# Performance work log

Hardware: AMD Instinct MI355X
Metric: run time of the kernel (lower is better)

Reference implementation:

```python
import jax, jax.numpy as jnp
import numpy as np

NHEADS = 8
START_ID = 1
MAX_LEN = 24

def _ln(x, g, b, eps=1e-5):
    m = x.mean(-1, keepdims=True)
    v = ((x - m) ** 2).mean(-1, keepdims=True)
    return (x - m) * jax.lax.rsqrt(v + eps) * g + b

def _mha(q_in, kv_in, w, b, ow, ob, mask):
    # q_in: [Lq,B,E], kv_in: [Lk,B,E]; w: [E,3E] packed q/k/v (transposed torch in_proj)
    E = q_in.shape[-1]; H = NHEADS; D = E // H
    Lq, B = q_in.shape[0], q_in.shape[1]; Lk = kv_in.shape[0]
    q = (q_in @ w[:, :E] + b[:E]).reshape(Lq, B, H, D)
    k = (kv_in @ w[:, E:2 * E] + b[E:2 * E]).reshape(Lk, B, H, D)
    v = (kv_in @ w[:, 2 * E:] + b[2 * E:]).reshape(Lk, B, H, D)
    s = jnp.einsum('qbhd,kbhd->bhqk', q, k) * (1.0 / float(np.sqrt(D)))
    if mask is not None:
        s = s + mask
    a = jax.nn.softmax(s, axis=-1)
    o = jnp.einsum('bhqk,kbhd->qbhd', a, v).reshape(Lq, B, E)
    return o @ ow + ob

def _sinusoidal_pe(S, E):
    pos = np.arange(S)[:, None]
    div = np.exp(np.arange(0, E, 2) * (-np.log(10000.0) / E))
    pe = np.zeros((S, E), dtype=np.float32)
    pe[:, 0::2] = np.sin(pos * div)
    pe[:, 1::2] = np.cos(pos * div)
    return jnp.asarray(pe)[:, None, :]  # [S,1,E]

def _model(input_tensor, emb, enc_attn_w, enc_attn_b, enc_attn_ow, enc_attn_ob,
           enc_ln1_g, enc_ln1_b, enc_ln2_g, enc_ln2_b,
           enc_ffn_w1, enc_ffn_b1, enc_ffn_w2, enc_ffn_b2,
           enc_norm_g, enc_norm_b,
           dec_sa_w, dec_sa_b, dec_sa_ow, dec_sa_ob,
           dec_ca_w, dec_ca_b, dec_ca_ow, dec_ca_ob,
           dec_ln1_g, dec_ln1_b, dec_ln2_g, dec_ln2_b, dec_ln3_g, dec_ln3_b,
           dec_ffn_w1, dec_ffn_b1, dec_ffn_w2, dec_ffn_b2,
           dec_norm_g, dec_norm_b, voc_w, voc_b):
    E = emb.shape[1]
    B, S = input_tensor.shape
    # encoder: seq-first [S,B,E], sinusoidal PE added (decoder side gets NO PE, as in source)
    x = jnp.take(emb, input_tensor.T, axis=0) + _sinusoidal_pe(S, E)
    for l in range(enc_attn_w.shape[0]):  # post-LN encoder layers
        a = _mha(x, x, enc_attn_w[l], enc_attn_b[l], enc_attn_ow[l], enc_attn_ob[l], None)
        x = _ln(x + a, enc_ln1_g[l], enc_ln1_b[l])
        f = jax.nn.relu(x @ enc_ffn_w1[l] + enc_ffn_b1[l]) @ enc_ffn_w2[l] + enc_ffn_b2[l]
        x = _ln(x + f, enc_ln2_g[l], enc_ln2_b[l])
    memory = _ln(x, enc_norm_g, enc_norm_b)

    Lbuf = MAX_LEN + 1
    causal = jnp.where(jnp.triu(jnp.ones((Lbuf, Lbuf), jnp.float32), k=1) == 1, -jnp.inf, 0.0)

    def dec_forward(tokens):
        # full (wasteful, KV-cache-free) decoder pass over the whole token buffer,
        # matching the source's recompute-everything greedy loop; causal masking
        # makes position i identical to the source's length-(i+1) prefix pass.
        y = jnp.take(emb, tokens, axis=0)  # [Lbuf,B,E]; shared embedding, no PE (as in source)
        for l in range(dec_sa_w.shape[0]):
            a = _mha(y, y, dec_sa_w[l], dec_sa_b[l], dec_sa_ow[l], dec_sa_ob[l], causal)
            y = _ln(y + a, dec_ln1_g[l], dec_ln1_b[l])
            c = _mha(y, memory, dec_ca_w[l], dec_ca_b[l], dec_ca_ow[l], dec_ca_ob[l], None)
            y = _ln(y + c, dec_ln2_g[l], dec_ln2_b[l])
            f = jax.nn.relu(y @ dec_ffn_w1[l] + dec_ffn_b1[l]) @ dec_ffn_w2[l] + dec_ffn_b2[l]
            y = _ln(y + f, dec_ln3_g[l], dec_ln3_b[l])
        return _ln(y, dec_norm_g, dec_norm_b)

    def step(tokens, i):
        out_i = jnp.take(dec_forward(tokens), i, axis=0)  # [B,E] == out[-1] of prefix pass
        prob = out_i @ voc_w + voc_b                      # [B,V_tgt]
        nxt = jnp.argmax(prob, axis=-1).astype(tokens.dtype)
        return tokens.at[i + 1].set(nxt), (nxt, prob)

    tokens0 = jnp.full((Lbuf, B), START_ID, dtype=input_tensor.dtype)
    _, (pred_tokens, dists) = jax.lax.scan(step, tokens0, jnp.arange(MAX_LEN))
    return pred_tokens, dists  # [MAX_LEN,B] int, [MAX_LEN,B,V_tgt]


def setup_inputs() -> dict:
    V, VT, E, F, LE, LD, B, S = 32000, 32000, 512, 2048, 3, 3, 8, 24
    keys = iter(jax.random.split(jax.random.key(0), 48))
    def W(*shape):
        return jax.random.normal(next(keys), shape, jnp.float32) * 0.02
    return dict(
        input_tensor=jax.random.randint(next(keys), (B, S), 0, V),
        emb=W(V, E),
        enc_attn_w=W(LE, E, 3 * E), enc_attn_b=jnp.zeros((LE, 3 * E)),
        enc_attn_ow=W(LE, E, E), enc_attn_ob=jnp.zeros((LE, E)),
        enc_ln1_g=jnp.ones((LE, E)), enc_ln1_b=jnp.zeros((LE, E)),
        enc_ln2_g=jnp.ones((LE, E)), enc_ln2_b=jnp.zeros((LE, E)),
        enc_ffn_w1=W(LE, E, F), enc_ffn_b1=jnp.zeros((LE, F)),
        enc_ffn_w2=W(LE, F, E), enc_ffn_b2=jnp.zeros((LE, E)),
        enc_norm_g=jnp.ones((E,)), enc_norm_b=jnp.zeros((E,)),
        dec_sa_w=W(LD, E, 3 * E), dec_sa_b=jnp.zeros((LD, 3 * E)),
        dec_sa_ow=W(LD, E, E), dec_sa_ob=jnp.zeros((LD, E)),
        dec_ca_w=W(LD, E, 3 * E), dec_ca_b=jnp.zeros((LD, 3 * E)),
        dec_ca_ow=W(LD, E, E), dec_ca_ob=jnp.zeros((LD, E)),
        dec_ln1_g=jnp.ones((LD, E)), dec_ln1_b=jnp.zeros((LD, E)),
        dec_ln2_g=jnp.ones((LD, E)), dec_ln2_b=jnp.zeros((LD, E)),
        dec_ln3_g=jnp.ones((LD, E)), dec_ln3_b=jnp.zeros((LD, E)),
        dec_ffn_w1=W(LD, E, F), dec_ffn_b1=jnp.zeros((LD, F)),
        dec_ffn_w2=W(LD, F, E), dec_ffn_b2=jnp.zeros((LD, E)),
        dec_norm_g=jnp.ones((E,)), dec_norm_b=jnp.zeros((E,)),
        voc_w=W(E, VT), voc_b=jnp.zeros((VT,)),
    )


def reference(input_tensor, emb, enc_attn_w, enc_attn_b, enc_attn_ow, enc_attn_ob,
              enc_ln1_g, enc_ln1_b, enc_ln2_g, enc_ln2_b,
              enc_ffn_w1, enc_ffn_b1, enc_ffn_w2, enc_ffn_b2,
              enc_norm_g, enc_norm_b,
              dec_sa_w, dec_sa_b, dec_sa_ow, dec_sa_ob,
              dec_ca_w, dec_ca_b, dec_ca_ow, dec_ca_ob,
              dec_ln1_g, dec_ln1_b, dec_ln2_g, dec_ln2_b, dec_ln3_g, dec_ln3_b,
              dec_ffn_w1, dec_ffn_b1, dec_ffn_w2, dec_ffn_b2,
              dec_norm_g, dec_norm_b, voc_w, voc_b):
    return _model(input_tensor, emb, enc_attn_w, enc_attn_b, enc_attn_ow, enc_attn_ob,
                  enc_ln1_g, enc_ln1_b, enc_ln2_g, enc_ln2_b,
                  enc_ffn_w1, enc_ffn_b1, enc_ffn_w2, enc_ffn_b2,
                  enc_norm_g, enc_norm_b,
                  dec_sa_w, dec_sa_b, dec_sa_ow, dec_sa_ob,
                  dec_ca_w, dec_ca_b, dec_ca_ow, dec_ca_ob,
                  dec_ln1_g, dec_ln1_b, dec_ln2_g, dec_ln2_b, dec_ln3_g, dec_ln3_b,
                  dec_ffn_w1, dec_ffn_b1, dec_ffn_w2, dec_ffn_b2,
                  dec_norm_g, dec_norm_b, voc_w, voc_b)
```

## Files before the change

kernel.cpp:

```cpp
#include <hip/hip_runtime.h>
#include <stdint.h>

#define E    512
#define H    8
#define DH   64
#define BB   8
#define SS   24
#define FF   2048
#define NL   3
#define VTOK 32000
#define LBUF 25
#define ML   24
#define START_ID 1

__global__ void enc_embed_kernel(const int* __restrict__ inp, const float* __restrict__ emb,
                                 float* __restrict__ x) {
  int r = blockIdx.x;
  int s = r / BB, b = r % BB;
  int tok = inp[b * SS + s];
  const float* er = emb + (size_t)tok * E;
  for (int e = threadIdx.x; e < E; e += blockDim.x) {
    int j = e >> 1;
    double dv = exp(-((double)(2 * j)) * (log(10000.0) / (double)E));
    double ang = (double)s * dv;
    double pe = (e & 1) ? cos(ang) : sin(ang);
    x[(size_t)r * E + e] = er[e] + (float)pe;
  }
}

__device__ __forceinline__ void ln_tile(float* Al, const float* __restrict__ g,
                                        const float* __restrict__ b,
                                        float* rm, float* rrs) {
  int t = threadIdx.x;
  int rr = t >> 5, q = t & 31;
  const float* ar = Al + rr * 512;
  float sm = 0.f, s2 = 0.f;
  for (int j = q; j < 512; j += 32) { float v = ar[j]; sm += v; s2 += v * v; }
  for (int off = 16; off; off >>= 1) {
    sm += __shfl_down(sm, off, 32);
    s2 += __shfl_down(s2, off, 32);
  }
  if (q == 0) {
    float m = sm * (1.0f / 512.0f);
    float var = s2 * (1.0f / 512.0f) - m * m;
    rm[rr] = m;
    rrs[rr] = 1.0f / sqrtf(var + 1e-5f);
  }
  __syncthreads();
  for (int idx = t; idx < 4096; idx += 256) {
    int r2 = idx >> 9, c2 = idx & 511;
    Al[idx] = (Al[idx] - rm[r2]) * rrs[r2] * g[c2] + b[c2];
  }
  __syncthreads();
}

__global__ __launch_bounds__(256) void fgemm_kernel(
    const float* __restrict__ A, int K,
    const float* __restrict__ W, int ldw, int N,
    const float* __restrict__ bias,
    const float* __restrict__ resid,
    float* __restrict__ C, int relu,
    unsigned long long* __restrict__ amax,
    const float* __restrict__ lng, const float* __restrict__ lnb,
    const float* __restrict__ lng2, const float* __restrict__ lnb2,
    float* __restrict__ astore,
    const int* __restrict__ gtok, const float* __restrict__ gemb,
    const float* __restrict__ rpart, const float* __restrict__ rbias,
    const float* __restrict__ rresid) {
  __shared__ float Al[8 * 512];
  __shared__ float red[16 * 512];
  __shared__ float rm[8], rrs[8];
  int t = threadIdx.x;
  int c0 = blockIdx.x * 64;
  int s = blockIdx.y;
  int row0 = blockIdx.z * 8;
  int kbase = s * 512;
  if (gtok) {
    for (int i = t; i < 1024; i += 256) {
      int r = i >> 7, cc = i & 127;
      int tok = gtok[r];
      ((float4*)Al)[i] = *(const float4*)(gemb + (size_t)tok * E + (cc << 2));
    }
  } else if (rpart) {
    for (int i = t; i < 1024; i += 256) {
      int r = i >> 7, cc = i & 127;
      int c = cc << 2;
      float4 v = *(const float4*)(rbias + c);
      float4 rv = *(const float4*)(rresid + (size_t)r * E + c);
      v.x += rv.x; v.y += rv.y; v.z += rv.z; v.w += rv.w;
      for (int sl = 0; sl < 4; ++sl) {
        float4 pv = *(const float4*)(rpart + ((size_t)sl * 8 + r) * E + c);
        v.x += pv.x; v.y += pv.y; v.z += pv.z; v.w += pv.w;
      }
      ((float4*)Al)[i] = v;
    }
  } else {
    for (int i = t; i < 1024; i += 256) {
      int r = i >> 7, cc = i & 127;
      ((float4*)Al)[i] = *(const float4*)(A + (size_t)(row0 + r) * K + kbase + (cc << 2));
    }
  }
  __syncthreads();
  if (lng) {
    ln_tile(Al, lng, lnb, rm, rrs);
    if (lng2) ln_tile(Al, lng2, lnb2, rm, rrs);
  }
  if (astore && blockIdx.x == 0 && blockIdx.y == 0) {
    float* ap = astore + (size_t)row0 * 512;
    for (int idx = t; idx < 4096; idx += 256) ap[idx] = Al[idx];
  }
  int tc = t & 15, tk = t >> 4;
  int col = c0 + (tc << 2);
  float acc[8][4];
#pragma unroll
  for (int m = 0; m < 8; ++m) { acc[m][0] = acc[m][1] = acc[m][2] = acc[m][3] = 0.f; }
  const float4* wp = (const float4*)(W + (size_t)kbase * ldw + col);
  const size_t ld4 = (size_t)(ldw >> 2);
#pragma unroll 8
  for (int i = 0; i < 32; ++i) {
    int k = tk + (i << 4);
    float4 wv = wp[(size_t)k * ld4];
#pragma unroll
    for (int m = 0; m < 8; ++m) {
      float a = Al[m * 512 + k];
      acc[m][0] += a * wv.x; acc[m][1] += a * wv.y;
      acc[m][2] += a * wv.z; acc[m][3] += a * wv.w;
    }
  }
#pragma unroll
  for (int m = 0; m < 8; ++m) {
    float4* rr2 = (float4*)&red[tk * 512 + m * 64 + (tc << 2)];
    *rr2 = make_float4(acc[m][0], acc[m][1], acc[m][2], acc[m][3]);
  }
  __syncthreads();
  float out2[2];
#pragma unroll
  for (int j = 0; j < 2; ++j) {
    int o = t + j * 256;
    float v = 0.f;
#pragma unroll
    for (int sl = 0; sl < 16; ++sl) v += red[sl * 512 + o];
    out2[j] = v;
  }
  int S = gridDim.y;
  if (S > 1) {
    int M = gridDim.z * 8;
#pragma unroll
    for (int j = 0; j < 2; ++j) {
      int o = t + j * 256; int m = o >> 6, cc = o & 63;
      C[((size_t)s * M + row0 + m) * N + c0 + cc] = out2[j];
    }
  } else {
#pragma unroll
    for (int j = 0; j < 2; ++j) {
      int o = t + j * 256; int m = o >> 6, cc = o & 63;
      int col2 = c0 + cc;
      float v = out2[j] + bias[col2];
      if (resid) v += resid[(size_t)(row0 + m) * N + col2];
      if (relu) v = fmaxf(v, 0.0f);
      C[(size_t)(row0 + m) * N + col2] = v;
      out2[j] = v;
    }
    if (amax) {
      __syncthreads();
      unsigned long long* keys = (unsigned long long*)red;
#pragma unroll
      for (int j = 0; j < 2; ++j) {
        int o = t + j * 256;
        unsigned int fb = __float_as_uint(out2[j]);
        fb = (fb & 0x80000000u) ? ~fb : (fb | 0x80000000u);
        int col2 = c0 + (o & 63);
        keys[o] = ((unsigned long long)fb << 32) |
                  (unsigned long long)(0xFFFFFFFFu - (unsigned)col2);
      }
      __syncthreads();
      if (t < 64) {
        for (int m = 0; m < 8; ++m) {
          unsigned long long k = keys[m * 64 + t];
          for (int off = 32; off; off >>= 1) {
            unsigned long long o2 = __shfl_down(k, off);
            if (o2 > k) k = o2;
          }
          if (t == 0) atomicMax(&amax[m], k);
        }
      }
    }
  }
}

__global__ __launch_bounds__(256) void reduce_br_kernel(const float* __restrict__ part, int S, int M,
                                 const float* __restrict__ bias,
                                 const float* __restrict__ resid,
                                 float* __restrict__ outp) {
  int r = blockIdx.x, t = threadIdx.x;
#pragma unroll
  for (int j = 0; j < 2; ++j) {
    int c = t + j * 256;
    float v = bias[c] + resid[(size_t)r * E + c];
    for (int s = 0; s < S; ++s) v += part[((size_t)s * M + r) * E + c];
    outp[(size_t)r * E + c] = v;
  }
}

__global__ __launch_bounds__(256) void reduce_ln_kernel(const float* __restrict__ part, int S,
                                 const float* __restrict__ bias,
                                 const float* __restrict__ resid,
                                 const float* __restrict__ g, const float* __restrict__ bta,
                                 float* __restrict__ out) {
  int b = blockIdx.x, t = threadIdx.x;
  float v0 = bias[t] + resid[(size_t)b * E + t];
  float v1 = bias[t + 256] + resid[(size_t)b * E + t + 256];
  for (int s = 0; s < S; ++s) {
    v0 += part[((size_t)s * 8 + b) * E + t];
    v1 += part[((size_t)s * 8 + b) * E + t + 256];
  }
  __shared__ float red[256];
  red[t] = v0 + v1;
  __syncthreads();
  for (int s = 128; s > 0; s >>= 1) { if (t < s) red[t] += red[t + s]; __syncthreads(); }
  float m = red[0] * (1.0f / (float)E);
  __syncthreads();
  float d0 = v0 - m, d1 = v1 - m;
  red[t] = d0 * d0 + d1 * d1;
  __syncthreads();
  for (int s = 128; s > 0; s >>= 1) { if (t < s) red[t] += red[t + s]; __syncthreads(); }
  float v = red[0] * (1.0f / (float)E);
  float rstd = 1.0f / sqrtf(v + 1e-5f);
  out[(size_t)b * E + t]       = d0 * rstd * g[t]       + bta[t];
  out[(size_t)b * E + t + 256] = d1 * rstd * g[t + 256] + bta[t + 256];
}

__global__ void enc_attn_kernel(const float* __restrict__ qkv, float* __restrict__ o) {
  int b = blockIdx.x >> 3, h = blockIdx.x & 7;
  __shared__ float qs[SS * DH], ks[SS * DH], vs[SS * DH];
  __shared__ float sc[SS][SS];
  int t = threadIdx.x;
  for (int idx = t; idx < SS * DH; idx += 256) {
    int srow = idx / DH, d = idx - srow * DH;
    size_t base = ((size_t)(srow * BB + b)) * (3 * E) + h * DH + d;
    qs[idx] = qkv[base];
    ks[idx] = qkv[base + E];
    vs[idx] = qkv[base + 2 * E];
  }
  __syncthreads();
  for (int p = t; p < SS * SS; p += 256) {
    int qi = p / SS, kj = p - qi * SS;
    float a = 0.f;
    for (int d = 0; d < DH; ++d) a += qs[qi * DH + d] * ks[kj * DH + d];
    sc[qi][kj] = a * 0.125f;
  }
  __syncthreads();
  if (t < SS) {
    float mx = -1e30f;
    for (int j = 0; j < SS; ++j) mx = fmaxf(mx, sc[t][j]);
    float sm = 0.f;
    for (int j = 0; j < SS; ++j) { float ev = expf(sc[t][j] - mx); sc[t][j] = ev; sm += ev; }
    float inv = 1.0f / sm;
    for (int j = 0; j < SS; ++j) sc[t][j] *= inv;
  }
  __syncthreads();
  for (int p = t; p < SS * DH; p += 256) {
    int qi = p / DH, d = p - qi * DH;
    float a = 0.f;
    for (int j = 0; j < SS; ++j) a += sc[qi][j] * vs[j * DH + d];
    o[((size_t)(qi * BB + b)) * E + h * DH + d] = a;
  }
}

__global__ __launch_bounds__(64) void dec_sa_attn_kernel(const float* __restrict__ qkv,
                                   float* __restrict__ Kc, float* __restrict__ Vc,
                                   float* __restrict__ o, int pos) {
  int b = blockIdx.x >> 3, h = blockIdx.x & 7;
  int t = threadIdx.x;
  const float* qp = qkv + (size_t)b * (3 * E) + h * DH;
  const float* kn = qp + E;
  const float* vn = qp + 2 * E;
  float* kc = Kc + ((size_t)pos * BB + b) * E + h * DH;
  float* vc = Vc + ((size_t)pos * BB + b) * E + h * DH;
  __shared__ float qs[DH];
  __shared__ float sc[32];
  kc[t] = kn[t]; vc[t] = vn[t]; qs[t] = qp[t];
  __syncthreads();
  int L = pos + 1;
  if (t < L) {
    const float* kr = (t == pos) ? kn : (Kc + ((size_t)t * BB + b) * E + h * DH);
    float a = 0.f;
#pragma unroll 8
    for (int d = 0; d < DH; ++d) a += qs[d] * kr[d];
    sc[t] = a * 0.125f;
  }
  __syncthreads();
  if (t == 0) {
    float mx = -1e30f;
    for (int j = 0; j < L; ++j) mx = fmaxf(mx, sc[j]);
    float sm = 0.f;
    for (int j = 0; j < L; ++j) { float ev = expf(sc[j] - mx); sc[j] = ev; sm += ev; }
    float inv = 1.0f / sm;
    for (int j = 0; j < L; ++j) sc[j] *= inv;
  }
  __syncthreads();
  float a = 0.f;
  for (int j = 0; j < L; ++j) {
    const float* vr = (j == pos) ? vn : (Vc + ((size_t)j * BB + b) * E + h * DH);
    a += sc[j] * vr[t];
  }
  o[(size_t)b * E + h * DH + t] = a;
}

__global__ __launch_bounds__(64) void dec_ca_attn_kernel(const float* __restrict__ q,
                                   const float* __restrict__ Km, const float* __restrict__ Vm,
                                   float* __restrict__ o) {
  int b = blockIdx.x >> 3, h = blockIdx.x & 7;
  int t = threadIdx.x;
  __shared__ float qs[DH];
  __shared__ float sc[SS];
  qs[t] = q[(size_t)b * E + h * DH + t];
  __syncthreads();
  if (t < SS) {
    const float* kr = Km + ((size_t)t * BB + b) * E + h * DH;
    float a = 0.f;
#pragma unroll 8
    for (int d = 0; d < DH; ++d) a += qs[d] * kr[d];
    sc[t] = a * 0.125f;
  }
  __syncthreads();
  if (t == 0) {
    float mx = -1e30f;
    for (int j = 0; j < SS; ++j) mx = fmaxf(mx, sc[j]);
    float sm = 0.f;
    for (int j = 0; j < SS; ++j) { float ev = expf(sc[j] - mx); sc[j] = ev; sm += ev; }
    float inv = 1.0f / sm;
    for (int j = 0; j < SS; ++j) sc[j] *= inv;
  }
  __syncthreads();
  float a = 0.f;
  for (int j = 0; j < SS; ++j) a += sc[j] * Vm[((size_t)j * BB + b) * E + h * DH + t];
  o[(size_t)b * E + h * DH + t] = a;
}

__global__ void dec_init_kernel(int* __restrict__ tokens, unsigned long long* __restrict__ amax) {
  int t = threadIdx.x;
  if (t < BB) { tokens[t] = START_ID; amax[t] = 0ull; }
}

__global__ void next_token_kernel(unsigned long long* __restrict__ amax, int* __restrict__ tokens,
                                  float* __restrict__ outtok, int i) {
  int t = threadIdx.x;
  if (t < BB) {
    unsigned long long p = amax[t];
    int idx = (int)(0xFFFFFFFFu - (unsigned int)(p & 0xFFFFFFFFull));
    tokens[(i + 1) * BB + t] = idx;
    outtok[i * BB + t] = (float)idx;
    amax[t] = 0ull;
  }
}

extern "C" void kernel_launch(void* const* d_in, const int* in_sizes, int n_in,
                              void* d_out, int out_size, void* d_ws, size_t ws_size,
                              hipStream_t stream) {
  (void)in_sizes; (void)n_in; (void)out_size; (void)ws_size;
  const int*   inp   = (const int*)d_in[0];
  const float* emb   = (const float*)d_in[1];
  const float* e_aw  = (const float*)d_in[2];
  const float* e_ab  = (const float*)d_in[3];
  const float* e_aow = (const float*)d_in[4];
  const float* e_aob = (const float*)d_in[5];
  const float* e_l1g = (const float*)d_in[6];
  const float* e_l1b = (const float*)d_in[7];
  const float* e_l2g = (const float*)d_in[8];
  const float* e_l2b = (const float*)d_in[9];
  const float* e_f1w = (const float*)d_in[10];
  const float* e_f1b = (const float*)d_in[11];
  const float* e_f2w = (const float*)d_in[12];
  const float* e_f2b = (const float*)d_in[13];
  const float* e_ng  = (const float*)d_in[14];
  const float* e_nb  = (const float*)d_in[15];
  const float* d_saw = (const float*)d_in[16];
  const float* d_sab = (const float*)d_in[17];
  const float* d_saow= (const float*)d_in[18];
  const float* d_saob= (const float*)d_in[19];
  const float* d_caw = (const float*)d_in[20];
  const float* d_cab = (const float*)d_in[21];
  const float* d_caow= (const float*)d_in[22];
  const float* d_caob= (const float*)d_in[23];
  const float* d_l1g = (const float*)d_in[24];
  const float* d_l1b = (const float*)d_in[25];
  const float* d_l2g = (const float*)d_in[26];
  const float* d_l2b = (const float*)d_in[27];
  const float* d_l3g = (const float*)d_in[28];
  const float* d_l3b = (const float*)d_in[29];
  const float* d_f1w = (const float*)d_in[30];
  const float* d_f1b = (const float*)d_in[31];
  const float* d_f2w = (const float*)d_in[32];
  const float* d_f2b = (const float*)d_in[33];
  const float* d_ng  = (const float*)d_in[34];
  const float* d_nb  = (const float*)d_in[35];
  const float* voc_w = (const float*)d_in[36];
  const float* voc_b = (const float*)d_in[37];
  float* out = (float*)d_out;

  float* p = (float*)d_ws;
  auto alloc = [&](size_t n) { float* r = p; p += n; return r; };
  float* enc_x   = alloc(192 * 512);
  float* enc_tmp = alloc(192 * 2048);
  float* enc_ao  = alloc(192 * 512);
  float* enc_raw = alloc(192 * 512);
  float* mem_k   = alloc(3 * 192 * 512);
  float* mem_v   = alloc(3 * 192 * 512);
  float* partE   = alloc(4 * 192 * 512);
  float* dqkv    = alloc(8 * 1536);
  float* y_in    = alloc(8 * 512);
  float* o_sa    = alloc(8 * 512);
  float* y1      = alloc(8 * 512);
  float* y1raw   = alloc(8 * 512);
  float* qca     = alloc(8 * 512);
  float* oca     = alloc(8 * 512);
  float* y2      = alloc(8 * 512);
  float* y2raw   = alloc(8 * 512);
  float* dmid    = alloc(8 * 2048);
  float* partD   = alloc(4 * 8 * 512);
  float* cacheK  = alloc(3 * LBUF * 8 * 512);
  float* cacheV  = alloc(3 * LBUF * 8 * 512);
  int* tokens    = (int*)alloc(LBUF * 8);
  unsigned long long* amax = (unsigned long long*)alloc(16);

#define FGZ nullptr, nullptr, nullptr, nullptr, nullptr, nullptr, nullptr, nullptr, nullptr, nullptr, nullptr

  enc_embed_kernel<<<dim3(192), dim3(256), 0, stream>>>(inp, emb, enc_x);
  for (int l = 0; l < NL; ++l) {
    const float* w  = e_aw  + (size_t)l * E * 3 * E;
    const float* bq = e_ab  + (size_t)l * 3 * E;
    if (l == 0) {
      fgemm_kernel<<<dim3(24, 1, 24), dim3(256), 0, stream>>>(
          enc_x, E, w, 3 * E, 3 * E, bq, nullptr, enc_tmp, 0, FGZ);
    } else {
      fgemm_kernel<<<dim3(24, 1, 24), dim3(256), 0, stream>>>(
          enc_raw, E, w, 3 * E, 3 * E, bq, nullptr, enc_tmp, 0,
          nullptr, e_l2g + (size_t)(l - 1) * E, e_l2b + (size_t)(l - 1) * E,
          nullptr, nullptr, enc_x,
          nullptr, nullptr, nullptr, nullptr, nullptr);
    }
    enc_attn_kernel<<<dim3(64), dim3(256), 0, stream>>>(enc_tmp, enc_ao);
    fgemm_kernel<<<dim3(8, 1, 24), dim3(256), 0, stream>>>(
        enc_ao, E, e_aow + (size_t)l * E * E, E, E, e_aob + (size_t)l * E,
        enc_x, enc_raw, 0, FGZ);
    fgemm_kernel<<<dim3(32, 1, 24), dim3(256), 0, stream>>>(
        enc_raw, E, e_f1w + (size_t)l * E * FF, FF, FF, e_f1b + (size_t)l * FF,
        nullptr, enc_tmp, 1,
        nullptr, e_l1g + (size_t)l * E, e_l1b + (size_t)l * E,
        nullptr, nullptr, enc_x,
        nullptr, nullptr, nullptr, nullptr, nullptr);
    fgemm_kernel<<<dim3(8, 4, 24), dim3(256), 0, stream>>>(
        enc_tmp, FF, e_f2w + (size_t)l * FF * E, E, E, nullptr,
        nullptr, partE, 0, FGZ);
    reduce_br_kernel<<<dim3(192), dim3(256), 0, stream>>>(
        partE, 4, 192, e_f2b + (size_t)l * E, enc_x, enc_raw);
  }

  for (int l = 0; l < NL; ++l) {
    const float* w  = d_caw + (size_t)l * E * 3 * E;
    const float* bq = d_cab + (size_t)l * 3 * E;
    fgemm_kernel<<<dim3(8, 1, 24), dim3(256), 0, stream>>>(
        enc_raw, E, w + E, 3 * E, E, bq + E, nullptr,
        mem_k + (size_t)l * 192 * 512, 0,
        nullptr, e_l2g + (size_t)2 * E, e_l2b + (size_t)2 * E,
        e_ng, e_nb, nullptr,
        nullptr, nullptr, nullptr, nullptr, nullptr);
    fgemm_kernel<<<dim3(8, 1, 24), dim3(256), 0, stream>>>(
        enc_raw, E, w + 2 * E, 3 * E, E, bq + 2 * E, nullptr,
        mem_v + (size_t)l * 192 * 512, 0,
        nullptr, e_l2g + (size_t)2 * E, e_l2b + (size_t)2 * E,
        e_ng, e_nb, nullptr,
        nullptr, nullptr, nullptr, nullptr, nullptr);
  }

  dec_init_kernel<<<dim3(1), dim3(64), 0, stream>>>(tokens, amax);
  for (int i = 0; i < ML; ++i) {
    for (int l = 0; l < NL; ++l) {
      const float* saw = d_saw + (size_t)l * E * 3 * E;
      const float* sab = d_sab + (size_t)l * 3 * E;
      const float* caw = d_caw + (size_t)l * E * 3 * E;
      const float* cab = d_cab + (size_t)l * 3 * E;
      float* Kc = cacheK + (size_t)l * LBUF * 8 * 512;
      float* Vc = cacheV + (size_t)l * LBUF * 8 * 512;

      if (l == 0) {
        fgemm_kernel<<<dim3(24, 1, 1), dim3(256), 0, stream>>>(
            nullptr, E, saw, 3 * E, 3 * E, sab, nullptr, dqkv, 0,
            nullptr, nullptr, nullptr, nullptr, nullptr, y_in,
            tokens + (size_t)i * BB, emb,
            nullptr, nullptr, nullptr);
      } else {
        fgemm_kernel<<<dim3(24, 1, 1), dim3(256), 0, stream>>>(
            nullptr, E, saw, 3 * E, 3 * E, sab, nullptr, dqkv, 0,
            nullptr, d_l3g + (size_t)(l - 1) * E, d_l3b + (size_t)(l - 1) * E,
            nullptr, nullptr, y_in,
            nullptr, nullptr,
            partD, d_f2b + (size_t)(l - 1) * E, y2);
      }
      dec_sa_attn_kernel<<<dim3(64), dim3(64), 0, stream>>>(dqkv, Kc, Vc, o_sa, i);
      fgemm_kernel<<<dim3(8, 1, 1), dim3(256), 0, stream>>>(
          o_sa, E, d_saow + (size_t)l * E * E, E, E, d_saob + (size_t)l * E,
          y_in, y1raw, 0, FGZ);
      fgemm_kernel<<<dim3(8, 1, 1), dim3(256), 0, stream>>>(
          y1raw, E, caw, 3 * E, E, cab, nullptr, qca, 0,
          nullptr, d_l1g + (size_t)l * E, d_l1b + (size_t)l * E,
          nullptr, nullptr, y1,
          nullptr, nullptr, nullptr, nullptr, nullptr);
      dec_ca_attn_kernel<<<dim3(64), dim3(64), 0, stream>>>(
          qca, mem_k + (size_t)l * 192 * 512, mem_v + (size_t)l * 192 * 512, oca);
      fgemm_kernel<<<dim3(8, 1, 1), dim3(256), 0, stream>>>(
          oca, E, d_caow + (size_t)l * E * E, E, E, d_caob + (size_t)l * E,
          y1, y2raw, 0, FGZ);
      fgemm_kernel<<<dim3(32, 1, 1), dim3(256), 0, stream>>>(
          y2raw, E, d_f1w + (size_t)l * E * FF, FF, FF, d_f1b + (size_t)l * FF,
          nullptr, dmid, 1,
          nullptr, d_l2g + (size_t)l * E, d_l2b + (size_t)l * E,
          nullptr, nullptr, y2,
          nullptr, nullptr, nullptr, nullptr, nullptr);
      fgemm_kernel<<<dim3(8, 4, 1), dim3(256), 0, stream>>>(
          dmid, FF, d_f2w + (size_t)l * FF * E, E, E, nullptr,
          nullptr, partD, 0, FGZ);
    }
    reduce_ln_kernel<<<dim3(8), dim3(256), 0, stream>>>(
        partD, 4, d_f2b + (size_t)(NL - 1) * E, y2,
        d_l3g + (size_t)(NL - 1) * E, d_l3b + (size_t)(NL - 1) * E, y_in);

    float* dist_i = out + 192 + (size_t)i * (8 * VTOK);
    fgemm_kernel<<<dim3(500, 1, 1), dim3(256), 0, stream>>>(
        y_in, E, voc_w, VTOK, VTOK, voc_b, nullptr, dist_i, 0,
        amax, d_ng, d_nb, nullptr, nullptr, nullptr,
        nullptr, nullptr, nullptr, nullptr, nullptr);
    next_token_kernel<<<dim3(1), dim3(64), 0, stream>>>(amax, tokens, out, i);
  }
#undef FGZ
}
```

Before: 6.219 ms.

## Fuse decoder attention with output projection via per-head partial sums

The decoder self- and cross-attention kernels now also apply the output projection, each head writing a partial product that the next GEMM's loader sums together with bias and residual before layernorm. This drops two fgemm launches per decoder layer and step, plus the intermediate buffers. The partial-sum loop count becomes a runtime parameter, and the fgemm inner-loop unroll rises from 8 to 16. In exchange, each attention block reads a 64x512 slice of the projection weight with only 64 blocks, so occupancy is low, and the next GEMM has to read 8 partial buffers.

```diff
diff --git a/kernel.cpp b/kernel.cpp
--- a/kernel.cpp
+++ b/kernel.cpp
@@ -66,7 +66,7 @@
     float* __restrict__ astore,
     const int* __restrict__ gtok, const float* __restrict__ gemb,
     const float* __restrict__ rpart, const float* __restrict__ rbias,
-    const float* __restrict__ rresid) {
+    const float* __restrict__ rresid, int rS) {
   __shared__ float Al[8 * 512];
   __shared__ float red[16 * 512];
   __shared__ float rm[8], rrs[8];
@@ -88,7 +88,7 @@
       float4 v = *(const float4*)(rbias + c);
       float4 rv = *(const float4*)(rresid + (size_t)r * E + c);
       v.x += rv.x; v.y += rv.y; v.z += rv.z; v.w += rv.w;
-      for (int sl = 0; sl < 4; ++sl) {
+      for (int sl = 0; sl < rS; ++sl) {
         float4 pv = *(const float4*)(rpart + ((size_t)sl * 8 + r) * E + c);
         v.x += pv.x; v.y += pv.y; v.z += pv.z; v.w += pv.w;
       }
@@ -116,7 +116,7 @@
   for (int m = 0; m < 8; ++m) { acc[m][0] = acc[m][1] = acc[m][2] = acc[m][3] = 0.f; }
   const float4* wp = (const float4*)(W + (size_t)kbase * ldw + col);
   const size_t ld4 = (size_t)(ldw >> 2);
-#pragma unroll 8
+#pragma unroll 16
   for (int i = 0; i < 32; ++i) {
     int k = tk + (i << 4);
     float4 wv = wp[(size_t)k * ld4];
@@ -267,26 +267,33 @@
   }
 }
 
-__global__ __launch_bounds__(64) void dec_sa_attn_kernel(const float* __restrict__ qkv,
-                                   float* __restrict__ Kc, float* __restrict__ Vc,
-                                   float* __restrict__ o, int pos) {
+__global__ __launch_bounds__(256) void dec_sa_part_kernel(
+    const float* __restrict__ qkv,
+    float* __restrict__ Kc, float* __restrict__ Vc, int pos,
+    const float* __restrict__ W,
+    float* __restrict__ part) {
   int b = blockIdx.x >> 3, h = blockIdx.x & 7;
   int t = threadIdx.x;
-  const float* qp = qkv + (size_t)b * (3 * E) + h * DH;
-  const float* kn = qp + E;
-  const float* vn = qp + 2 * E;
-  float* kc = Kc + ((size_t)pos * BB + b) * E + h * DH;
-  float* vc = Vc + ((size_t)pos * BB + b) * E + h * DH;
-  __shared__ float qs[DH];
+  __shared__ float qs[DH], os[DH];
   __shared__ float sc[32];
-  kc[t] = kn[t]; vc[t] = vn[t]; qs[t] = qp[t];
+  const float* base = qkv + (size_t)b * 1536 + h * DH;
+  if (t < DH) {
+    qs[t] = base[t];
+    Kc[((size_t)pos * BB + b) * E + h * DH + t] = base[512 + t];
+    Vc[((size_t)pos * BB + b) * E + h * DH + t] = base[1024 + t];
+  }
   __syncthreads();
   int L = pos + 1;
   if (t < L) {
-    const float* kr = (t == pos) ? kn : (Kc + ((size_t)t * BB + b) * E + h * DH);
+    const float4* k4 = (t == pos) ? (const float4*)(base + 512)
+                                  : (const float4*)(Kc + ((size_t)t * BB + b) * E + h * DH);
+    const float4* q4 = (const float4*)qs;
     float a = 0.f;
-#pragma unroll 8
-    for (int d = 0; d < DH; ++d) a += qs[d] * kr[d];
+#pragma unroll
+    for (int d = 0; d < 16; ++d) {
+      float4 qv = q4[d], kv = k4[d];
+      a += qv.x * kv.x + qv.y * kv.y + qv.z * kv.z + qv.w * kv.w;
+    }
     sc[t] = a * 0.125f;
   }
   __syncthreads();
@@ -299,28 +306,48 @@
     for (int j = 0; j < L; ++j) sc[j] *= inv;
   }
   __syncthreads();
-  float a = 0.f;
-  for (int j = 0; j < L; ++j) {
-    const float* vr = (j == pos) ? vn : (Vc + ((size_t)j * BB + b) * E + h * DH);
-    a += sc[j] * vr[t];
-  }
-  o[(size_t)b * E + h * DH + t] = a;
-}
-
-__global__ __launch_bounds__(64) void dec_ca_attn_kernel(const float* __restrict__ q,
-                                   const float* __restrict__ Km, const float* __restrict__ Vm,
-                                   float* __restrict__ o) {
+  if (t < DH) {
+    float a = 0.f;
+    for (int j = 0; j < L; ++j) {
+      float vv = (j == pos) ? base[1024 + t]
+                            : Vc[((size_t)j * BB + b) * E + h * DH + t];
+      a += sc[j] * vv;
+    }
+    os[t] = a;
+  }
+  __syncthreads();
+  float p0 = 0.f, p1 = 0.f;
+  const float* wr = W + (size_t)h * DH * E;
+#pragma unroll 8
+  for (int d = 0; d < DH; ++d) {
+    float o = os[d];
+    p0 += o * wr[(size_t)d * E + t];
+    p1 += o * wr[(size_t)d * E + t + 256];
+  }
+  float* pp = part + ((size_t)h * BB + b) * E;
+  pp[t] = p0; pp[t + 256] = p1;
+}
+
+__global__ __launch_bounds__(256) void dec_ca_part_kernel(
+    const float* __restrict__ q,
+    const float* __restrict__ Km, const float* __restrict__ Vm,
+    const float* __restrict__ W,
+    float* __restrict__ part) {
   int b = blockIdx.x >> 3, h = blockIdx.x & 7;
   int t = threadIdx.x;
-  __shared__ float qs[DH];
+  __shared__ float qs[DH], os[DH];
   __shared__ float sc[SS];
-  qs[t] = q[(size_t)b * E + h * DH + t];
+  if (t < DH) qs[t] = q[(size_t)b * E + h * DH + t];
   __syncthreads();
   if (t < SS) {
-    const float* kr = Km + ((size_t)t * BB + b) * E + h * DH;
+    const float4* k4 = (const float4*)(Km + ((size_t)t * BB + b) * E + h * DH);
+    const float4* q4 = (const float4*)qs;
     float a = 0.f;
-#pragma unroll 8
-    for (int d = 0; d < DH; ++d) a += qs[d] * kr[d];
+#pragma unroll
+    for (int d = 0; d < 16; ++d) {
+      float4 qv = q4[d], kv = k4[d];
+      a += qv.x * kv.x + qv.y * kv.y + qv.z * kv.z + qv.w * kv.w;
+    }
     sc[t] = a * 0.125f;
   }
   __syncthreads();
@@ -333,9 +360,23 @@
     for (int j = 0; j < SS; ++j) sc[j] *= inv;
   }
   __syncthreads();
-  float a = 0.f;
-  for (int j = 0; j < SS; ++j) a += sc[j] * Vm[((size_t)j * BB + b) * E + h * DH + t];
-  o[(size_t)b * E + h * DH + t] = a;
+  if (t < DH) {
+    float a = 0.f;
+    for (int j = 0; j < SS; ++j)
+      a += sc[j] * Vm[((size_t)j * BB + b) * E + h * DH + t];
+    os[t] = a;
+  }
+  __syncthreads();
+  float p0 = 0.f, p1 = 0.f;
+  const float* wr = W + (size_t)h * DH * E;
+#pragma unroll 8
+  for (int d = 0; d < DH; ++d) {
+    float o = os[d];
+    p0 += o * wr[(size_t)d * E + t];
+    p1 += o * wr[(size_t)d * E + t + 256];
+  }
+  float* pp = part + ((size_t)h * BB + b) * E;
+  pp[t] = p0; pp[t + 256] = p1;
 }
 
 __global__ void dec_init_kernel(int* __restrict__ tokens, unsigned long long* __restrict__ amax) {
@@ -410,21 +451,19 @@
   float* partE   = alloc(4 * 192 * 512);
   float* dqkv    = alloc(8 * 1536);
   float* y_in    = alloc(8 * 512);
-  float* o_sa    = alloc(8 * 512);
   float* y1      = alloc(8 * 512);
-  float* y1raw   = alloc(8 * 512);
+  float* y2      = alloc(8 * 512);
   float* qca     = alloc(8 * 512);
-  float* oca     = alloc(8 * 512);
-  float* y2      = alloc(8 * 512);
-  float* y2raw   = alloc(8 * 512);
   float* dmid    = alloc(8 * 2048);
   float* partD   = alloc(4 * 8 * 512);
+  float* partSA  = alloc(8 * 8 * 512);
+  float* partCA  = alloc(8 * 8 * 512);
   float* cacheK  = alloc(3 * LBUF * 8 * 512);
   float* cacheV  = alloc(3 * LBUF * 8 * 512);
   int* tokens    = (int*)alloc(LBUF * 8);
   unsigned long long* amax = (unsigned long long*)alloc(16);
 
-#define FGZ nullptr, nullptr, nullptr, nullptr, nullptr, nullptr, nullptr, nullptr, nullptr, nullptr, nullptr
+#define FGZ nullptr, nullptr, nullptr, nullptr, nullptr, nullptr, nullptr, nullptr, nullptr, nullptr, nullptr, 0
 
   enc_embed_kernel<<<dim3(192), dim3(256), 0, stream>>>(inp, emb, enc_x);
   for (int l = 0; l < NL; ++l) {
@@ -438,7 +477,7 @@
           enc_raw, E, w, 3 * E, 3 * E, bq, nullptr, enc_tmp, 0,
           nullptr, e_l2g + (size_t)(l - 1) * E, e_l2b + (size_t)(l - 1) * E,
           nullptr, nullptr, enc_x,
-          nullptr, nullptr, nullptr, nullptr, nullptr);
+          nullptr, nullptr, nullptr, nullptr, nullptr, 0);
     }
     enc_attn_kernel<<<dim3(64), dim3(256), 0, stream>>>(enc_tmp, enc_ao);
     fgemm_kernel<<<dim3(8, 1, 24), dim3(256), 0, stream>>>(
@@ -449,7 +488,7 @@
         nullptr, enc_tmp, 1,
         nullptr, e_l1g + (size_t)l * E, e_l1b + (size_t)l * E,
         nullptr, nullptr, enc_x,
-        nullptr, nullptr, nullptr, nullptr, nullptr);
+        nullptr, nullptr, nullptr, nullptr, nullptr, 0);
     fgemm_kernel<<<dim3(8, 4, 24), dim3(256), 0, stream>>>(
         enc_tmp, FF, e_f2w + (size_t)l * FF * E, E, E, nullptr,
         nullptr, partE, 0, FGZ);
@@ -465,13 +504,13 @@
         mem_k + (size_t)l * 192 * 512, 0,
         nullptr, e_l2g + (size_t)2 * E, e_l2b + (size_t)2 * E,
         e_ng, e_nb, nullptr,
-        nullptr, nullptr, nullptr, nullptr, nullptr);
+        nullptr, nullptr, nullptr, nullptr, nullptr, 0);
     fgemm_kernel<<<dim3(8, 1, 24), dim3(256), 0, stream>>>(
         enc_raw, E, w + 2 * E, 3 * E, E, bq + 2 * E, nullptr,
         mem_v + (size_t)l * 192 * 512, 0,
         nullptr, e_l2g + (size_t)2 * E, e_l2b + (size_t)2 * E,
         e_ng, e_nb, nullptr,
-        nullptr, nullptr, nullptr, nullptr, nullptr);
+        nullptr, nullptr, nullptr, nullptr, nullptr, 0);
   }
 
   dec_init_kernel<<<dim3(1), dim3(64), 0, stream>>>(tokens, amax);
@@ -489,35 +528,33 @@
             nullptr, E, saw, 3 * E, 3 * E, sab, nullptr, dqkv, 0,
             nullptr, nullptr, nullptr, nullptr, nullptr, y_in,
             tokens + (size_t)i * BB, emb,
-            nullptr, nullptr, nullptr);
+            nullptr, nullptr, nullptr, 0);
       } else {
         fgemm_kernel<<<dim3(24, 1, 1), dim3(256), 0, stream>>>(
             nullptr, E, saw, 3 * E, 3 * E, sab, nullptr, dqkv, 0,
             nullptr, d_l3g + (size_t)(l - 1) * E, d_l3b + (size_t)(l - 1) * E,
             nullptr, nullptr, y_in,
             nullptr, nullptr,
-            partD, d_f2b + (size_t)(l - 1) * E, y2);
+            partD, d_f2b + (size_t)(l - 1) * E, y2, 4);
       }
-      dec_sa_attn_kernel<<<dim3(64), dim3(64), 0, stream>>>(dqkv, Kc, Vc, o_sa, i);
+      dec_sa_part_kernel<<<dim3(64), dim3(256), 0, stream>>>(
+          dqkv, Kc, Vc, i, d_saow + (size_t)l * E * E, partSA);
       fgemm_kernel<<<dim3(8, 1, 1), dim3(256), 0, stream>>>(
-          o_sa, E, d_saow + (size_t)l * E * E, E, E, d_saob + (size_t)l * E,
-          y_in, y1raw, 0, FGZ);
-      fgemm_kernel<<<dim3(8, 1, 1), dim3(256), 0, stream>>>(
-          y1raw, E, caw, 3 * E, E, cab, nullptr, qca, 0,
+          nullptr, E, caw, 3 * E, E, cab, nullptr, qca, 0,
           nullptr, d_l1g + (size_t)l * E, d_l1b + (size_t)l * E,
           nullptr, nullptr, y1,
-          nullptr, nullptr, nullptr, nullptr, nullptr);
-      dec_ca_attn_kernel<<<dim3(64), dim3(64), 0, stream>>>(
-          qca, mem_k + (size_t)l * 192 * 512, mem_v + (size_t)l * 192 * 512, oca);
-      fgemm_kernel<<<dim3(8, 1, 1), dim3(256), 0, stream>>>(
-          oca, E, d_caow + (size_t)l * E * E, E, E, d_caob + (size_t)l * E,
-          y1, y2raw, 0, FGZ);
+          nullptr, nullptr,
+          partSA, d_saob + (size_t)l * E, y_in, 8);
+      dec_ca_part_kernel<<<dim3(64), dim3(256), 0, stream>>>(
+          qca, mem_k + (size_t)l * 192 * 512, mem_v + (size_t)l * 192 * 512,
+          d_caow + (size_t)l * E * E, partCA);
       fgemm_kernel<<<dim3(32, 1, 1), dim3(256), 0, stream>>>(
-          y2raw, E, d_f1w + (size_t)l * E * FF, FF, FF, d_f1b + (size_t)l * FF,
+          nullptr, E, d_f1w + (size_t)l * E * FF, FF, FF, d_f1b + (size_t)l * FF,
           nullptr, dmid, 1,
           nullptr, d_l2g + (size_t)l * E, d_l2b + (size_t)l * E,
           nullptr, nullptr, y2,
-          nullptr, nullptr, nullptr, nullptr, nullptr);
+          nullptr, nullptr,
+          partCA, d_caob + (size_t)l * E, y1, 8);
       fgemm_kernel<<<dim3(8, 4, 1), dim3(256), 0, stream>>>(
           dmid, FF, d_f2w + (size_t)l * FF * E, E, E, nullptr,
           nullptr, partD, 0, FGZ);
@@ -530,7 +567,7 @@
     fgemm_kernel<<<dim3(500, 1, 1), dim3(256), 0, stream>>>(
         y_in, E, voc_w, VTOK, VTOK, voc_b, nullptr, dist_i, 0,
         amax, d_ng, d_nb, nullptr, nullptr, nullptr,
-        nullptr, nullptr, nullptr, nullptr, nullptr);
+        nullptr, nullptr, nullptr, nullptr, nullptr, 0);
     next_token_kernel<<<dim3(1), dim3(64), 0, stream>>>(amax, tokens, out, i);
   }
 #undef FGZ
```

Measured after the change: 7.268 ms. +16.9%, slower.
